# Kernel optimization log

Hardware: AMD Instinct MI355X
Metric: run time of the kernel (lower is better)

## Reference

```python
import jax, jax.numpy as jnp
import numpy as np

EMBED_DIM = 1024
NUM_HEADS = 16
HEAD_DIM = EMBED_DIM // NUM_HEADS


def setup_inputs() -> dict:
    key = jax.random.key(0)
    kx, kq, kk, kv = jax.random.split(key, 4)
    x = jax.random.normal(kx, (4, 2048, EMBED_DIM), dtype=jnp.float32)
    s = 1.0 / np.sqrt(EMBED_DIM)
    # nn.Linear weight layout: [out, in]; y = x @ W.T
    w_q = jax.random.uniform(kq, (EMBED_DIM, EMBED_DIM), jnp.float32, -s, s)
    w_k = jax.random.uniform(kk, (EMBED_DIM, EMBED_DIM), jnp.float32, -s, s)
    w_v = jax.random.uniform(kv, (EMBED_DIM, EMBED_DIM), jnp.float32, -s, s)
    return {"x": x, "w_q": w_q, "w_k": w_k, "w_v": w_v}


def reference(x, w_q, w_k, w_v):
    B, S, E = x.shape
    H, D = NUM_HEADS, HEAD_DIM
    # projections (Linear without bias): x @ W.T, split into heads
    q = (x @ w_q.T).reshape(B, S, H, D).transpose(0, 2, 1, 3)  # [B,H,S,D]
    k = (x @ w_k.T).reshape(B, S, H, D).transpose(0, 2, 1, 3)  # [B,H,S,D]
    v = (x @ w_v.T).reshape(B, S, H, D).transpose(0, 2, 1, 3)  # [B,H,S,D]
    # NOTE: original scales by sqrt(embed_dim), not sqrt(head_dim)
    scores = jnp.einsum('bhqd,bhkd->bhqk', q, k) / jnp.sqrt(jnp.float32(E))
    attn = jax.nn.softmax(scores, axis=-1)
    out = jnp.einsum('bhqk,bhkd->bhqd', attn, v)
    # concat heads; original forward never applies fc_out
    return out.transpose(0, 2, 1, 3).reshape(B, S, E)
```

## Files before the change

kernel.cpp:

```cpp
#include <hip/hip_runtime.h>
#include <hip/hip_bf16.h>

typedef __hip_bfloat16 bf16;
typedef float f32x4 __attribute__((ext_vector_type(4)));
typedef short bf16x8 __attribute__((ext_vector_type(8)));
typedef short bf16x4 __attribute__((ext_vector_type(4)));
typedef unsigned u32x4 __attribute__((ext_vector_type(4)));

#define DI __device__ __forceinline__

constexpr int B_ = 4, S_ = 2048, E_ = 1024, H_ = 16, D_ = 64;
constexpr int M_ = B_ * S_;
constexpr float QSCALE = 0.03125f * 1.4426950408889634f;

DI unsigned short bfbits(float f) {
  __hip_bfloat16 h = __float2bfloat16(f);
  return *reinterpret_cast<unsigned short*>(&h);
}

DI unsigned cvt_pk_bf16(float lo, float hi) {
  unsigned r;
  asm("v_cvt_pk_bf16_f32 %0, %1, %2" : "=v"(r) : "v"(lo), "v"(hi));
  return r;
}

DI void gload_lds16(const bf16* g, bf16* l) {
  __builtin_amdgcn_global_load_lds((const __attribute__((address_space(1))) void*)g,
                                   (__attribute__((address_space(3))) void*)l, 16, 0, 0);
}

__global__ __launch_bounds__(256) void cast_all(const float* __restrict__ x,
                                                const float* __restrict__ wq,
                                                const float* __restrict__ wk,
                                                const float* __restrict__ wv,
                                                ushort* __restrict__ xb,
                                                ushort* __restrict__ wqb,
                                                ushort* __restrict__ wkb,
                                                ushort* __restrict__ wvb) {
  int id = blockIdx.x * 256 + threadIdx.x;
  const float* src; ushort* dst; int i;
  if (id < 2097152)      { src = x;  dst = xb;  i = id; }
  else if (id < 2359296) { src = wq; dst = wqb; i = id - 2097152; }
  else if (id < 2621440) { src = wk; dst = wkb; i = id - 2359296; }
  else                   { src = wv; dst = wvb; i = id - 2621440; }
  float4 v = reinterpret_cast<const float4*>(src)[i];
  ushort4 o;
  o.x = bfbits(v.x); o.y = bfbits(v.y); o.z = bfbits(v.z); o.w = bfbits(v.w);
  reinterpret_cast<ushort4*>(dst)[i] = o;
}

__global__ __launch_bounds__(512, 2) void gemm_qkv_8ph(const bf16* __restrict__ A,
                                                       const bf16* __restrict__ W,
                                                       bf16* __restrict__ Qh,
                                                       bf16* __restrict__ Kh,
                                                       bf16* __restrict__ Vth) {
  constexpr int NG = E_ / 32;
  __shared__ __align__(16) bf16 lds[65536];
  const int t = threadIdx.x, l = t & 63, w = t >> 6;
  const int hi = l >> 4, r15 = l & 15;
  const int wm = w >> 2, wn = w & 3;

  const int bid = blockIdx.x;
  const int swz = (bid & 7) * 48 + (bid >> 3);
  const int mt = swz / 12, nt = swz - mt * 12;
  const int m0 = mt * 256, n0 = nt * 256;

  f32x4 acc[8][4] = {};

  auto stageM = [&](int g, int kind) {
    const bf16* src = (kind == 0) ? A + (size_t)m0 * E_ : W + (size_t)n0 * E_;
    bf16* base = lds + (size_t)(g & 3) * 16384 + kind * 8192 + (w * 64) * 8;
#pragma unroll
    for (int i2 = 0; i2 < 2; ++i2) {
      int gr = i2 * 512 + t;
      int row = gr >> 2, slot = gr & 3;
      int ch = slot ^ (row & 3);
      gload_lds16(src + (size_t)row * E_ + g * 32 + ch * 8, base + i2 * 4096);
    }
  };

  stageM(0, 0); stageM(0, 1);
  stageM(1, 0); stageM(1, 1);
  asm volatile("s_waitcnt vmcnt(4)" ::: "memory");
  __builtin_amdgcn_s_barrier();

  for (int g = 0; g < NG; ++g) {
    const char* sa = (const char*)(lds + (size_t)(g & 3) * 16384);
    const char* sb = sa + 8192 * 2;
    bf16x8 bfrag[4];
#pragma unroll
    for (int mg = 0; mg < 2; ++mg) {
      bf16x8 afrag[4];
#pragma unroll
      for (int mm = 0; mm < 4; ++mm) {
        int row = wm * 128 + (mg * 4 + mm) * 16 + r15;
        afrag[mm] = *(const bf16x8*)(sa + row * 64 + ((hi ^ (row & 3)) * 16));
      }
      if (mg == 0) {
#pragma unroll
        for (int nf = 0; nf < 4; ++nf) {
          int row = wn * 64 + nf * 16 + r15;
          bfrag[nf] = *(const bf16x8*)(sb + row * 64 + ((hi ^ (row & 3)) * 16));
        }
      }
      if (g < NG - 2) stageM(g + 2, mg);
      __builtin_amdgcn_s_barrier();
      asm volatile("s_waitcnt lgkmcnt(0)" ::: "memory");
      __builtin_amdgcn_sched_barrier(0);
      __builtin_amdgcn_s_setprio(1);
#pragma unroll
      for (int mm = 0; mm < 4; ++mm)
#pragma unroll
        for (int nf = 0; nf < 4; ++nf)
          acc[mg * 4 + mm][nf] =
              __builtin_amdgcn_mfma_f32_16x16x32_bf16(afrag[mm], bfrag[nf],
                                                      acc[mg * 4 + mm][nf], 0, 0, 0);
      __builtin_amdgcn_s_setprio(0);
      if (mg == 1) {
        if (g < NG - 2)       asm volatile("s_waitcnt vmcnt(4)" ::: "memory");
        else if (g == NG - 2) asm volatile("s_waitcnt vmcnt(0)" ::: "memory");
      }
      __builtin_amdgcn_s_barrier();
    }
  }

  const int ncol0 = n0 + wn * 64;
  const int sec = ncol0 >> 10;
  const int h = (ncol0 >> 6) & 15;
  const int mrow = m0 + wm * 128;
  const int b = mrow >> 11, sbase = mrow & 2047;
  char* wb = (char*)lds + w * 16384;

  if (sec < 2) {
    bf16* dst = sec == 0 ? Qh : Kh;
    const float osc = sec == 0 ? QSCALE : 1.0f;
#pragma unroll
    for (int mf = 0; mf < 8; ++mf)
#pragma unroll
      for (int nf = 0; nf < 4; ++nf)
#pragma unroll
        for (int jj = 0; jj < 4; ++jj) {
          int s = mf * 16 + 4 * hi + jj;
          int d = nf * 16 + r15;
          *(bf16*)(wb + s * 128 + ((d * 2) ^ ((s & 7) << 4))) =
              __float2bfloat16(acc[mf][nf][jj] * osc);
        }
    asm volatile("s_waitcnt lgkmcnt(0)" ::: "memory");
    __builtin_amdgcn_sched_barrier(0);
    bf16* obase = dst + ((size_t)(b * H_ + h) * S_ + sbase) * D_;
#pragma unroll
    for (int c = 0; c < 16; ++c) {
      int s = c * 8 + (l >> 3), dch = l & 7;
      bf16x8 v = *(const bf16x8*)(wb + s * 128 + ((dch * 16) ^ ((s & 7) << 4)));
      *(bf16x8*)(obase + (size_t)s * D_ + dch * 8) = v;
    }
  } else {
#pragma unroll
    for (int mf = 0; mf < 8; ++mf)
#pragma unroll
      for (int nf = 0; nf < 4; ++nf)
#pragma unroll
        for (int m2 = 0; m2 < 2; ++m2) {
          int s = mf * 16 + 4 * hi + m2 * 2;
          int d = nf * 16 + r15;
          unsigned u = cvt_pk_bf16(acc[mf][nf][m2 * 2], acc[mf][nf][m2 * 2 + 1]);
          *(unsigned*)(wb + d * 256 + ((s * 2) ^ ((d & 7) << 4))) = u;
        }
    asm volatile("s_waitcnt lgkmcnt(0)" ::: "memory");
    __builtin_amdgcn_sched_barrier(0);
    const int d = l;
    bf16* obase = Vth + ((size_t)(b * H_ + h) * D_ + d) * S_ + sbase;
#pragma unroll
    for (int c = 0; c < 16; ++c) {
      bf16x8 v = *(const bf16x8*)(wb + d * 256 + ((c * 16) ^ ((d & 7) << 4)));
      *(bf16x8*)(obase + c * 8) = v;
    }
  }
}

__global__ __launch_bounds__(256) void attn_kernel(const bf16* __restrict__ Q,
                                                   const bf16* __restrict__ K,
                                                   const bf16* __restrict__ Vt,
                                                   float* __restrict__ out) {
  constexpr int KT = 64, NT = S_ / KT;
  __shared__ __align__(16) bf16 Ks[2][KT * D_];
  __shared__ __align__(16) bf16 Vs[2][D_ * KT];

  const int t = threadIdx.x, l = t & 63, w = t >> 6;
  const int hi = l >> 4, r15 = l & 15;
  const int p = blockIdx.x;
  const int lg = (p & 7) * 256 + (p >> 3);
  const int qblk = lg & 31, h = (lg >> 5) & 15, b = lg >> 9;
  const int q0 = qblk * 64 + w * 16;
  const size_t bh = (size_t)(b * H_ + h);
  const bf16* Qb = Q + bh * S_ * D_;
  const bf16* Kb = K + bh * S_ * D_;
  const bf16* Vb = Vt + bh * D_ * S_;

  bf16x8 aq[2];
#pragma unroll
  for (int c = 0; c < 2; ++c)
    aq[c] = *reinterpret_cast<const bf16x8*>(Qb + (size_t)(q0 + r15) * D_ + c * 32 + hi * 8);

  int koff[2][4], voff[2][4][2];
#pragma unroll
  for (int c = 0; c < 2; ++c)
#pragma unroll
    for (int nt = 0; nt < 4; ++nt) {
      int r = nt * 16 + r15;
      koff[c][nt] = (r * D_ + ((4 * c + hi) ^ (r & 7)) * 8) * 2;
      int d = nt * 16 + r15;
#pragma unroll
      for (int hf = 0; hf < 2; ++hf) {
        int blk = 4 * c + 2 * hf + (hi >> 1);
        voff[c][nt][hf] = (d * KT + ((blk ^ (d & 7)) * 8) + 4 * (hi & 1)) * 2;
      }
    }

  f32x4 o_acc[4] = {};
  float lsum = 0.f;

  auto stage = [&](int buf, int kt) {
    const bf16* Kt_ = Kb + (size_t)kt * KT * D_;
    const bf16* Vt_ = Vb + kt * KT;
#pragma unroll
    for (int i = 0; i < 2; ++i) {
      int idx = i * 256 + t;
      int rr = idx >> 3, s = idx & 7;
      int g = s ^ (rr & 7);
      gload_lds16(Kt_ + rr * D_ + g * 8, &Ks[buf][(i * 256 + w * 64) * 8]);
      gload_lds16(Vt_ + (size_t)rr * S_ + g * 8, &Vs[buf][(i * 256 + w * 64) * 8]);
    }
  };

  auto tile = [&](int buf) {
    const char* kbase = (const char*)Ks[buf];
    const char* vbase = (const char*)Vs[buf];
    f32x4 sc[4] = {};
#pragma unroll
    for (int c = 0; c < 2; ++c)
#pragma unroll
      for (int nt = 0; nt < 4; ++nt) {
        bf16x8 bk = *reinterpret_cast<const bf16x8*>(kbase + koff[c][nt]);
        sc[nt] = __builtin_amdgcn_mfma_f32_16x16x32_bf16(bk, aq[c], sc[nt], 0, 0, 0);
      }
    u32x4 pa[2];
#pragma unroll
    for (int nt = 0; nt < 4; ++nt) {
      float pf0 = __builtin_amdgcn_exp2f(sc[nt][0]);
      float pf1 = __builtin_amdgcn_exp2f(sc[nt][1]);
      float pf2 = __builtin_amdgcn_exp2f(sc[nt][2]);
      float pf3 = __builtin_amdgcn_exp2f(sc[nt][3]);
      lsum += (pf0 + pf1) + (pf2 + pf3);
      pa[nt >> 1][(nt & 1) * 2 + 0] = cvt_pk_bf16(pf0, pf1);
      pa[nt >> 1][(nt & 1) * 2 + 1] = cvt_pk_bf16(pf2, pf3);
    }
#pragma unroll
    for (int c = 0; c < 2; ++c) {
      bf16x8 ap = __builtin_bit_cast(bf16x8, pa[c]);
#pragma unroll
      for (int nt = 0; nt < 4; ++nt) {
        bf16x4 v0 = *reinterpret_cast<const bf16x4*>(vbase + voff[c][nt][0]);
        bf16x4 v1 = *reinterpret_cast<const bf16x4*>(vbase + voff[c][nt][1]);
        bf16x8 bv;
#pragma unroll
        for (int e = 0; e < 4; ++e) { bv[e] = v0[e]; bv[e + 4] = v1[e]; }
        o_acc[nt] = __builtin_amdgcn_mfma_f32_16x16x32_bf16(ap, bv, o_acc[nt], 0, 0, 0);
      }
    }
  };

  stage(0, 0);
  for (int kt = 0; kt < NT; kt += 2) {
    __syncthreads();
    if (kt + 1 < NT) stage(1, kt + 1);
    tile(0);
    __syncthreads();
    if (kt + 2 < NT) stage(0, kt + 2);
    tile(1);
  }

  lsum += __shfl_xor(lsum, 16);
  lsum += __shfl_xor(lsum, 32);
  float inv = 1.f / lsum;
#pragma unroll
  for (int jj = 0; jj < 4; ++jj) {
    float invj = __shfl(inv, (l & 48) + hi * 4 + jj);
    int q = q0 + hi * 4 + jj;
#pragma unroll
    for (int nt = 0; nt < 4; ++nt) {
      int d = nt * 16 + r15;
      out[((size_t)b * S_ + q) * E_ + h * D_ + d] = o_acc[nt][jj] * invj;
    }
  }
}

extern "C" void kernel_launch(void* const* d_in, const int* in_sizes, int n_in,
                              void* d_out, int out_size, void* d_ws, size_t ws_size,
                              hipStream_t stream) {
  const float* x = (const float*)d_in[0];
  const float* wq = (const float*)d_in[1];
  const float* wk = (const float*)d_in[2];
  const float* wv = (const float*)d_in[3];
  float* out = (float*)d_out;
  char* ws = (char*)d_ws;

  bf16* xb  = (bf16*)(ws + 0);
  bf16* wqb = (bf16*)(ws + 16777216);
  bf16* wkb = (bf16*)(ws + 18874368);
  bf16* wvb = (bf16*)(ws + 20971520);
  bf16* Qh  = (bf16*)(ws + 23068672);
  bf16* Kh  = (bf16*)(ws + 39845888);
  bf16* Vth = (bf16*)(ws + 56623104);

  cast_all<<<11264, 256, 0, stream>>>(x, wq, wk, wv, (ushort*)xb, (ushort*)wqb,
                                      (ushort*)wkb, (ushort*)wvb);

  gemm_qkv_8ph<<<384, 512, 0, stream>>>(xb, wqb, Qh, Kh, Vth);

  attn_kernel<<<2048, 256, 0, stream>>>(Qh, Kh, Vth, out);
}
```

Baseline: 265.3 us.

## Double Q rows per attention wave, deepen GEMM prefetch, remap GEMM tiles

The attention kernel now has each wave handle 32 query rows instead of 16, so each K/V tile loaded into LDS feeds twice as many MFMAs, and the grid is halved to 1024 blocks. The QKV GEMM gains a third prefetch stage with matching vmcnt waits, a new XCD-aware tile mapping, and a different LDS swizzle pattern. Together these aim to cut LDS and global traffic per FLOP and to hide load latency better. The cost is higher register pressure and fewer attention blocks, which may lower occupancy.

```diff
diff --git a/kernel.cpp b/kernel.cpp
--- a/kernel.cpp
+++ b/kernel.cpp
@@ -61,8 +61,9 @@
   const int wm = w >> 2, wn = w & 3;
 
   const int bid = blockIdx.x;
-  const int swz = (bid & 7) * 48 + (bid >> 3);
-  const int mt = swz / 12, nt = swz - mt * 12;
+  const int xcd = bid & 7, j = bid >> 3;
+  const int mt = (xcd >> 1) * 8 + (j & 7);
+  const int nt = (xcd & 1) * 6 + (j >> 3);
   const int m0 = mt * 256, n0 = nt * 256;
 
   f32x4 acc[8][4] = {};
@@ -74,14 +75,15 @@
     for (int i2 = 0; i2 < 2; ++i2) {
       int gr = i2 * 512 + t;
       int row = gr >> 2, slot = gr & 3;
-      int ch = slot ^ (row & 3);
+      int ch = slot ^ ((row >> 1) & 3);
       gload_lds16(src + (size_t)row * E_ + g * 32 + ch * 8, base + i2 * 4096);
     }
   };
 
   stageM(0, 0); stageM(0, 1);
   stageM(1, 0); stageM(1, 1);
-  asm volatile("s_waitcnt vmcnt(4)" ::: "memory");
+  stageM(2, 0); stageM(2, 1);
+  asm volatile("s_waitcnt vmcnt(8)" ::: "memory");
   __builtin_amdgcn_s_barrier();
 
   for (int g = 0; g < NG; ++g) {
@@ -94,16 +96,16 @@
 #pragma unroll
       for (int mm = 0; mm < 4; ++mm) {
         int row = wm * 128 + (mg * 4 + mm) * 16 + r15;
-        afrag[mm] = *(const bf16x8*)(sa + row * 64 + ((hi ^ (row & 3)) * 16));
+        afrag[mm] = *(const bf16x8*)(sa + row * 64 + ((hi ^ ((row >> 1) & 3)) * 16));
       }
       if (mg == 0) {
 #pragma unroll
         for (int nf = 0; nf < 4; ++nf) {
           int row = wn * 64 + nf * 16 + r15;
-          bfrag[nf] = *(const bf16x8*)(sb + row * 64 + ((hi ^ (row & 3)) * 16));
+          bfrag[nf] = *(const bf16x8*)(sb + row * 64 + ((hi ^ ((row >> 1) & 3)) * 16));
         }
       }
-      if (g < NG - 2) stageM(g + 2, mg);
+      if (g < NG - 3) stageM(g + 3, mg);
       __builtin_amdgcn_s_barrier();
       asm volatile("s_waitcnt lgkmcnt(0)" ::: "memory");
       __builtin_amdgcn_sched_barrier(0);
@@ -117,7 +119,8 @@
                                                       acc[mg * 4 + mm][nf], 0, 0, 0);
       __builtin_amdgcn_s_setprio(0);
       if (mg == 1) {
-        if (g < NG - 2)       asm volatile("s_waitcnt vmcnt(4)" ::: "memory");
+        if (g < NG - 3)       asm volatile("s_waitcnt vmcnt(8)" ::: "memory");
+        else if (g == NG - 3) asm volatile("s_waitcnt vmcnt(4)" ::: "memory");
         else if (g == NG - 2) asm volatile("s_waitcnt vmcnt(0)" ::: "memory");
       }
       __builtin_amdgcn_s_barrier();
@@ -189,36 +192,38 @@
   const int t = threadIdx.x, l = t & 63, w = t >> 6;
   const int hi = l >> 4, r15 = l & 15;
   const int p = blockIdx.x;
-  const int lg = (p & 7) * 256 + (p >> 3);
-  const int qblk = lg & 31, h = (lg >> 5) & 15, b = lg >> 9;
-  const int q0 = qblk * 64 + w * 16;
+  const int lg = (p & 7) * 128 + (p >> 3);
+  const int qblk = lg & 15, h = (lg >> 4) & 15, b = lg >> 8;
+  const int q0 = qblk * 128 + w * 32;
   const size_t bh = (size_t)(b * H_ + h);
   const bf16* Qb = Q + bh * S_ * D_;
   const bf16* Kb = K + bh * S_ * D_;
   const bf16* Vb = Vt + bh * D_ * S_;
 
-  bf16x8 aq[2];
+  bf16x8 aq0[2], aq1[2];
+#pragma unroll
+  for (int c = 0; c < 2; ++c) {
+    aq0[c] = *reinterpret_cast<const bf16x8*>(Qb + (size_t)(q0 + r15) * D_ + c * 32 + hi * 8);
+    aq1[c] = *reinterpret_cast<const bf16x8*>(Qb + (size_t)(q0 + 16 + r15) * D_ + c * 32 + hi * 8);
+  }
+
+  int koff[2][4], voff[2][4][2];
 #pragma unroll
   for (int c = 0; c < 2; ++c)
-    aq[c] = *reinterpret_cast<const bf16x8*>(Qb + (size_t)(q0 + r15) * D_ + c * 32 + hi * 8);
-
-  int koff[2][4], voff[2][4][2];
-#pragma unroll
-  for (int c = 0; c < 2; ++c)
-#pragma unroll
-    for (int nt = 0; nt < 4; ++nt) {
-      int r = nt * 16 + r15;
-      koff[c][nt] = (r * D_ + ((4 * c + hi) ^ (r & 7)) * 8) * 2;
-      int d = nt * 16 + r15;
+#pragma unroll
+    for (int n4 = 0; n4 < 4; ++n4) {
+      int r = n4 * 16 + r15;
+      koff[c][n4] = (r * D_ + ((4 * c + hi) ^ (r & 7)) * 8) * 2;
+      int d = n4 * 16 + r15;
 #pragma unroll
       for (int hf = 0; hf < 2; ++hf) {
         int blk = 4 * c + 2 * hf + (hi >> 1);
-        voff[c][nt][hf] = (d * KT + ((blk ^ (d & 7)) * 8) + 4 * (hi & 1)) * 2;
-      }
-    }
-
-  f32x4 o_acc[4] = {};
-  float lsum = 0.f;
+        voff[c][n4][hf] = (d * KT + ((blk ^ (d & 7)) * 8) + 4 * (hi & 1)) * 2;
+      }
+    }
+
+  f32x4 o_acc0[4] = {}, o_acc1[4] = {};
+  float lsum0 = 0.f, lsum1 = 0.f;
 
   auto stage = [&](int buf, int kt) {
     const bf16* Kt_ = Kb + (size_t)kt * KT * D_;
@@ -236,36 +241,46 @@
   auto tile = [&](int buf) {
     const char* kbase = (const char*)Ks[buf];
     const char* vbase = (const char*)Vs[buf];
-    f32x4 sc[4] = {};
+    f32x4 sc0[4] = {}, sc1[4] = {};
 #pragma unroll
     for (int c = 0; c < 2; ++c)
 #pragma unroll
-      for (int nt = 0; nt < 4; ++nt) {
-        bf16x8 bk = *reinterpret_cast<const bf16x8*>(kbase + koff[c][nt]);
-        sc[nt] = __builtin_amdgcn_mfma_f32_16x16x32_bf16(bk, aq[c], sc[nt], 0, 0, 0);
-      }
-    u32x4 pa[2];
-#pragma unroll
-    for (int nt = 0; nt < 4; ++nt) {
-      float pf0 = __builtin_amdgcn_exp2f(sc[nt][0]);
-      float pf1 = __builtin_amdgcn_exp2f(sc[nt][1]);
-      float pf2 = __builtin_amdgcn_exp2f(sc[nt][2]);
-      float pf3 = __builtin_amdgcn_exp2f(sc[nt][3]);
-      lsum += (pf0 + pf1) + (pf2 + pf3);
-      pa[nt >> 1][(nt & 1) * 2 + 0] = cvt_pk_bf16(pf0, pf1);
-      pa[nt >> 1][(nt & 1) * 2 + 1] = cvt_pk_bf16(pf2, pf3);
+      for (int n4 = 0; n4 < 4; ++n4) {
+        bf16x8 bk = *reinterpret_cast<const bf16x8*>(kbase + koff[c][n4]);
+        sc0[n4] = __builtin_amdgcn_mfma_f32_16x16x32_bf16(bk, aq0[c], sc0[n4], 0, 0, 0);
+        sc1[n4] = __builtin_amdgcn_mfma_f32_16x16x32_bf16(bk, aq1[c], sc1[n4], 0, 0, 0);
+      }
+    u32x4 pa0[2], pa1[2];
+#pragma unroll
+    for (int n4 = 0; n4 < 4; ++n4) {
+      float a0 = __builtin_amdgcn_exp2f(sc0[n4][0]);
+      float a1 = __builtin_amdgcn_exp2f(sc0[n4][1]);
+      float a2 = __builtin_amdgcn_exp2f(sc0[n4][2]);
+      float a3 = __builtin_amdgcn_exp2f(sc0[n4][3]);
+      lsum0 += (a0 + a1) + (a2 + a3);
+      pa0[n4 >> 1][(n4 & 1) * 2 + 0] = cvt_pk_bf16(a0, a1);
+      pa0[n4 >> 1][(n4 & 1) * 2 + 1] = cvt_pk_bf16(a2, a3);
+      float b0 = __builtin_amdgcn_exp2f(sc1[n4][0]);
+      float b1 = __builtin_amdgcn_exp2f(sc1[n4][1]);
+      float b2 = __builtin_amdgcn_exp2f(sc1[n4][2]);
+      float b3 = __builtin_amdgcn_exp2f(sc1[n4][3]);
+      lsum1 += (b0 + b1) + (b2 + b3);
+      pa1[n4 >> 1][(n4 & 1) * 2 + 0] = cvt_pk_bf16(b0, b1);
+      pa1[n4 >> 1][(n4 & 1) * 2 + 1] = cvt_pk_bf16(b2, b3);
     }
 #pragma unroll
     for (int c = 0; c < 2; ++c) {
-      bf16x8 ap = __builtin_bit_cast(bf16x8, pa[c]);
-#pragma unroll
-      for (int nt = 0; nt < 4; ++nt) {
-        bf16x4 v0 = *reinterpret_cast<const bf16x4*>(vbase + voff[c][nt][0]);
-        bf16x4 v1 = *reinterpret_cast<const bf16x4*>(vbase + voff[c][nt][1]);
+      bf16x8 ap0 = __builtin_bit_cast(bf16x8, pa0[c]);
+      bf16x8 ap1 = __builtin_bit_cast(bf16x8, pa1[c]);
+#pragma unroll
+      for (int n4 = 0; n4 < 4; ++n4) {
+        bf16x4 v0 = *reinterpret_cast<const bf16x4*>(vbase + voff[c][n4][0]);
+        bf16x4 v1 = *reinterpret_cast<const bf16x4*>(vbase + voff[c][n4][1]);
         bf16x8 bv;
 #pragma unroll
         for (int e = 0; e < 4; ++e) { bv[e] = v0[e]; bv[e + 4] = v1[e]; }
-        o_acc[nt] = __builtin_amdgcn_mfma_f32_16x16x32_bf16(ap, bv, o_acc[nt], 0, 0, 0);
+        o_acc0[n4] = __builtin_amdgcn_mfma_f32_16x16x32_bf16(ap0, bv, o_acc0[n4], 0, 0, 0);
+        o_acc1[n4] = __builtin_amdgcn_mfma_f32_16x16x32_bf16(ap1, bv, o_acc1[n4], 0, 0, 0);
       }
     }
   };
@@ -280,17 +295,22 @@
     tile(1);
   }
 
-  lsum += __shfl_xor(lsum, 16);
-  lsum += __shfl_xor(lsum, 32);
-  float inv = 1.f / lsum;
+  lsum0 += __shfl_xor(lsum0, 16);
+  lsum0 += __shfl_xor(lsum0, 32);
+  lsum1 += __shfl_xor(lsum1, 16);
+  lsum1 += __shfl_xor(lsum1, 32);
+  float inv0 = 1.f / lsum0, inv1 = 1.f / lsum1;
 #pragma unroll
   for (int jj = 0; jj < 4; ++jj) {
-    float invj = __shfl(inv, (l & 48) + hi * 4 + jj);
-    int q = q0 + hi * 4 + jj;
-#pragma unroll
-    for (int nt = 0; nt < 4; ++nt) {
-      int d = nt * 16 + r15;
-      out[((size_t)b * S_ + q) * E_ + h * D_ + d] = o_acc[nt][jj] * invj;
+    float i0 = __shfl(inv0, (l & 48) + hi * 4 + jj);
+    float i1 = __shfl(inv1, (l & 48) + hi * 4 + jj);
+    int qa = q0 + hi * 4 + jj;
+    int qb2 = q0 + 16 + hi * 4 + jj;
+#pragma unroll
+    for (int n4 = 0; n4 < 4; ++n4) {
+      int d = n4 * 16 + r15;
+      out[((size_t)b * S_ + qa) * E_ + h * D_ + d] = o_acc0[n4][jj] * i0;
+      out[((size_t)b * S_ + qb2) * E_ + h * D_ + d] = o_acc1[n4][jj] * i1;
     }
   }
 }
@@ -318,5 +338,5 @@
 
   gemm_qkv_8ph<<<384, 512, 0, stream>>>(xb, wqb, Qh, Kh, Vth);
 
-  attn_kernel<<<2048, 256, 0, stream>>>(Qh, Kh, Vth, out);
-}
+  attn_kernel<<<1024, 256, 0, stream>>>(Qh, Kh, Vth, out);
+}
```

Result: faster. 245.3 us (-7.5%).
